# Performance work log

Measured on AMD Instinct MI355X. Metric: run time of the kernel, lower is better.

Reference implementation:

```python
import jax, jax.numpy as jnp
import numpy as np

B, N, D = 2, 2048, 1024
H, HD = 16, 64


def setup_inputs() -> dict:
    key = jax.random.key(0)
    ks = jax.random.split(key, 5)
    return {
        "hidden_states": jax.random.normal(ks[0], (B, N, D), dtype=jnp.float32),
        "W_attn": jax.random.normal(ks[1], (D, 3 * D), dtype=jnp.float32) * (D ** -0.5),
        "b_attn": jax.random.normal(ks[2], (3 * D,), dtype=jnp.float32) * 0.02,
        "W_proj": jax.random.normal(ks[3], (D, D), dtype=jnp.float32) * (D ** -0.5),
        "b_proj": jax.random.normal(ks[4], (D,), dtype=jnp.float32) * 0.02,
    }


def reference(hidden_states, W_attn, b_attn, W_proj, b_proj):
    # QKV projection: [B,N,3D]
    proj = hidden_states @ W_attn + b_attn
    q, k, v = jnp.split(proj, 3, axis=-1)
    # [B,N,H,HD]
    q = q.reshape(B, N, H, HD)
    k = k.reshape(B, N, H, HD)
    v = v.reshape(B, N, H, HD)
    scale = HD ** -0.5
    # naive attention: full [B,H,Nq,Nkv] score matrix
    attn = jnp.einsum("bqhd,bkhd->bhqk", q, k) * scale
    q_pos = jnp.arange(N)
    kv_pos = jnp.arange(N)
    # mask where kv_pos > start_pos + q_pos (start_pos = 0)
    mask = kv_pos[None, :] > q_pos[:, None]  # [Nq, Nkv]
    attn = jnp.where(mask[None, None, :, :], -jnp.inf, attn)
    attn = jax.nn.softmax(attn, axis=-1)
    out = jnp.einsum("bhqk,bkhd->bqhd", attn, v)  # [B,N,H,HD]
    out = out.reshape(B, N, D)
    return out @ W_proj + b_proj
```

## Files before the change

### kernel.cpp

```cpp
#include <hip/hip_runtime.h>
#include <hip/hip_bf16.h>

#define BB 2
#define NN 2048
#define DDIM 1024
#define HH 16
#define HDD 64

typedef __attribute__((ext_vector_type(8))) short bf16x8;
typedef __attribute__((ext_vector_type(4))) short bf16x4;
typedef __attribute__((ext_vector_type(4))) float f32x4;

__device__ inline ushort f2bf(float x) {
  __hip_bfloat16 h = __float2bfloat16(x);
  ushort u;
  __builtin_memcpy(&u, &h, 2);
  return u;
}

#define GLOAD_LDS16(g, l)                                                            \
  __builtin_amdgcn_global_load_lds((const __attribute__((address_space(1))) void*)(g), \
                                   (__attribute__((address_space(3))) void*)(l), 16, 0, 0)

__global__ __launch_bounds__(256) void cvt_f32_bf16(const float* __restrict__ in,
                                                    ushort* __restrict__ out, int n4) {
  int i = blockIdx.x * 256 + threadIdx.x;
  if (i >= n4) return;
  float4 a = ((const float4*)in)[i];
  ushort4 o;
  o.x = f2bf(a.x); o.y = f2bf(a.y); o.z = f2bf(a.z); o.w = f2bf(a.w);
  ((ushort4*)out)[i] = o;
}

__global__ __launch_bounds__(256) void transpose_cvt(const float* __restrict__ in,
                                                     ushort* __restrict__ out, int R, int C) {
  __shared__ float tile[32][33];
  int bx = blockIdx.x * 32, by = blockIdx.y * 32;
  int tx = threadIdx.x, ty = threadIdx.y;
#pragma unroll
  for (int r = ty; r < 32; r += 8)
    tile[r][tx] = in[(size_t)(by + r) * C + bx + tx];
  __syncthreads();
#pragma unroll
  for (int r = ty; r < 32; r += 8)
    out[(size_t)(bx + r) * R + by + tx] = f2bf(tile[tx][r]);
}

template <int MODE>
__global__ __launch_bounds__(256) void gemm_bt(const ushort* __restrict__ A,
                                               const ushort* __restrict__ Bt,
                                               const float* __restrict__ bias,
                                               void* __restrict__ Cv,
                                               ushort* __restrict__ Vt,
                                               int M, int N, int K) {
  __shared__ ushort As[128 * 32];
  __shared__ ushort Bs[128 * 32];
  const int tid = threadIdx.x;
  const int wid = tid >> 6, lane = tid & 63;
  const int c = lane & 15, g = lane >> 4;
  const int wm = (wid >> 1) * 64, wn = (wid & 1) * 64;
  const int m0 = blockIdx.y * 128, n0 = blockIdx.x * 128;
  f32x4 acc[4][4] = {};
  for (int k0 = 0; k0 < K; k0 += 32) {
    __syncthreads();
#pragma unroll
    for (int it = 0; it < 2; ++it) {
      int G = tid + it * 256;
      int row = G >> 2, sl = G & 3;
      GLOAD_LDS16(A + (size_t)(m0 + row) * K + k0 + sl * 8, &As[G * 8]);
      GLOAD_LDS16(Bt + (size_t)(n0 + row) * K + k0 + sl * 8, &Bs[G * 8]);
    }
    __syncthreads();
    bf16x8 af[4], bfr[4];
#pragma unroll
    for (int i = 0; i < 4; ++i) {
      af[i] = *(const bf16x8*)(&As[(wm + i * 16 + c) * 32 + g * 8]);
      bfr[i] = *(const bf16x8*)(&Bs[(wn + i * 16 + c) * 32 + g * 8]);
    }
#pragma unroll
    for (int i = 0; i < 4; ++i)
#pragma unroll
      for (int j = 0; j < 4; ++j)
        acc[i][j] = __builtin_amdgcn_mfma_f32_16x16x32_bf16(af[i], bfr[j], acc[i][j], 0, 0, 0);
  }
#pragma unroll
  for (int i = 0; i < 4; ++i) {
#pragma unroll
    for (int j = 0; j < 4; ++j) {
      const int col = n0 + wn + j * 16 + c;
      const float bv = bias[col];
      const int row = m0 + wm + i * 16 + g * 4;
      if (MODE == 2 && col >= 2048) {
        const int hh = (col - 2048) >> 6, dd = (col - 2048) & 63;
        const int bb = row >> 11, nl = row & 2047;
        ushort4 ov;
        ov.x = f2bf(acc[i][j][0] + bv);
        ov.y = f2bf(acc[i][j][1] + bv);
        ov.z = f2bf(acc[i][j][2] + bv);
        ov.w = f2bf(acc[i][j][3] + bv);
        *(ushort4*)(&Vt[(size_t)((bb * 16 + hh) * 64 + dd) * NN + nl]) = ov;
      } else {
        const int ldc = (MODE == 2) ? 2048 : N;
#pragma unroll
        for (int ri = 0; ri < 4; ++ri) {
          float v = acc[i][j][ri] + bv;
          if (MODE == 0)
            ((float*)Cv)[(size_t)(row + ri) * ldc + col] = v;
          else
            ((ushort*)Cv)[(size_t)(row + ri) * ldc + col] = f2bf(v);
        }
      }
    }
  }
}

__global__ __launch_bounds__(256) void attn_fwd(const ushort* __restrict__ QK,
                                                const ushort* __restrict__ Vt,
                                                ushort* __restrict__ O) {
  const int bh = blockIdx.x;
  const int b = bh >> 4, h = bh & 15;
  const int qb = (int)gridDim.y - 1 - (int)blockIdx.y;
  const int tid = threadIdx.x;
  const int wid = tid >> 6, lane = tid & 63;
  const int c = lane & 15, g = lane >> 4;
  const int q0 = qb * 64 + wid * 16;
  const ushort* Qb = QK + (size_t)b * NN * 2048 + (size_t)h * HDD;
  const ushort* Kb = Qb + 1024;
  const ushort* Vb = Vt + (size_t)bh * HDD * NN;

  __shared__ ushort Ks[64 * 64];
  __shared__ ushort Vs[64 * 64];

  bf16x8 qf[2];
  {
    const ushort* qrow = Qb + (size_t)(q0 + c) * 2048 + g * 8;
    qf[0] = *(const bf16x8*)(qrow);
    qf[1] = *(const bf16x8*)(qrow + 32);
  }
  f32x4 oacc[4] = {};
  float m = -INFINITY, lsum = 0.f;
  const int q_abs = q0 + c;
  const int ntiles = qb + 1;

  for (int t = 0; t < ntiles; ++t) {
    const int kv0 = t * 64;
    __syncthreads();
#pragma unroll
    for (int it = 0; it < 2; ++it) {
      int u = tid + it * 256;
      int row = u >> 3, sl = u & 7;
      *(bf16x8*)(&Ks[row * 64 + ((sl ^ (row & 7)) * 8)]) =
          *(const bf16x8*)(Kb + (size_t)(kv0 + row) * 2048 + sl * 8);
      *(bf16x8*)(&Vs[row * 64 + ((sl ^ (row & 7)) * 8)]) =
          *(const bf16x8*)(Vb + (size_t)row * NN + kv0 + sl * 8);
    }
    __syncthreads();

    f32x4 s[4] = {};
#pragma unroll
    for (int f = 0; f < 4; ++f) {
      int krow = f * 16 + c;
#pragma unroll
      for (int dc = 0; dc < 2; ++dc) {
        int slot = dc * 4 + g;
        bf16x8 kf = *(const bf16x8*)(&Ks[krow * 64 + ((slot ^ (krow & 7)) * 8)]);
        s[f] = __builtin_amdgcn_mfma_f32_16x16x32_bf16(kf, qf[dc], s[f], 0, 0, 0);
      }
    }

    float pmax = -INFINITY;
#pragma unroll
    for (int f = 0; f < 4; ++f)
#pragma unroll
      for (int i = 0; i < 4; ++i) {
        int kv_abs = kv0 + f * 16 + g * 4 + i;
        float sv = (kv_abs > q_abs) ? -INFINITY : s[f][i] * 0.125f;
        s[f][i] = sv;
        pmax = fmaxf(pmax, sv);
      }
    pmax = fmaxf(pmax, __shfl_xor(pmax, 16));
    pmax = fmaxf(pmax, __shfl_xor(pmax, 32));
    float mnew = fmaxf(m, pmax);
    float corr = __expf(m - mnew);
    float psum = 0.f;
#pragma unroll
    for (int f = 0; f < 4; ++f)
#pragma unroll
      for (int i = 0; i < 4; ++i) {
        float p = __expf(s[f][i] - mnew);
        s[f][i] = p;
        psum += p;
      }
    psum += __shfl_xor(psum, 16);
    psum += __shfl_xor(psum, 32);
    lsum = lsum * corr + psum;
    m = mnew;
#pragma unroll
    for (int db = 0; db < 4; ++db) {
      oacc[db][0] *= corr; oacc[db][1] *= corr;
      oacc[db][2] *= corr; oacc[db][3] *= corr;
    }

#pragma unroll
    for (int f = 0; f < 4; ++f) {
      bf16x4 pb;
      pb[0] = (short)f2bf(s[f][0]);
      pb[1] = (short)f2bf(s[f][1]);
      pb[2] = (short)f2bf(s[f][2]);
      pb[3] = (short)f2bf(s[f][3]);
      const int slot = f * 2 + (g >> 1);
#pragma unroll
      for (int db = 0; db < 4; ++db) {
        int d = db * 16 + c;
        bf16x4 vf = *(const bf16x4*)(&Vs[d * 64 + ((slot ^ (d & 7)) * 8) + (g & 1) * 4]);
        oacc[db] = __builtin_amdgcn_mfma_f32_16x16x16bf16_1k(vf, pb, oacc[db], 0, 0, 0);
      }
    }
  }

  float invl = 1.f / lsum;
  ushort* orow = O + (size_t)(b * NN + q0 + c) * DDIM + h * HDD;
#pragma unroll
  for (int db = 0; db < 4; ++db) {
    ushort4 ov;
    ov.x = f2bf(oacc[db][0] * invl);
    ov.y = f2bf(oacc[db][1] * invl);
    ov.z = f2bf(oacc[db][2] * invl);
    ov.w = f2bf(oacc[db][3] * invl);
    *(ushort4*)(&orow[db * 16 + g * 4]) = ov;
  }
}

extern "C" void kernel_launch(void* const* d_in, const int* in_sizes, int n_in,
                              void* d_out, int out_size, void* d_ws, size_t ws_size,
                              hipStream_t stream) {
  const float* hidden = (const float*)d_in[0];
  const float* W_attn = (const float*)d_in[1];
  const float* b_attn = (const float*)d_in[2];
  const float* W_proj = (const float*)d_in[3];
  const float* b_proj = (const float*)d_in[4];

  char* ws = (char*)d_ws;
  ushort* hbf  = (ushort*)(ws);
  ushort* WaT  = (ushort*)(ws + (size_t)(8 << 20));
  ushort* WpT  = (ushort*)(ws + (size_t)(14 << 20));
  ushort* qk   = (ushort*)(ws + (size_t)(16 << 20));
  ushort* vt   = (ushort*)(ws + (size_t)(32 << 20));
  ushort* aout = (ushort*)(ws + (size_t)(40 << 20));

  cvt_f32_bf16<<<4096, 256, 0, stream>>>(hidden, hbf, (BB * NN * DDIM) / 4);
  transpose_cvt<<<dim3(96, 32), dim3(32, 8), 0, stream>>>(W_attn, WaT, 1024, 3072);
  transpose_cvt<<<dim3(32, 32), dim3(32, 8), 0, stream>>>(W_proj, WpT, 1024, 1024);

  gemm_bt<2><<<dim3(24, 32), 256, 0, stream>>>(hbf, WaT, b_attn, qk, vt, 4096, 3072, 1024);
  attn_fwd<<<dim3(32, 32), 256, 0, stream>>>(qk, vt, aout);
  gemm_bt<0><<<dim3(8, 32), 256, 0, stream>>>(aout, WpT, b_proj, d_out, nullptr, 4096, 1024, 1024);
}
```

Measured before the change: 230.1 us.

## Double-buffer attention K/V via direct LDS loads, lazy softmax rescale, new proj GEMM

The attention kernel now double-buffers K/V tiles in LDS using global_load_lds, so the next tile loads while the current one is computed, and drops one barrier per iteration. The softmax folds scale·log2e into Q, uses raw exp2, applies the causal mask only on the diagonal tile, skips rescaling unless the running max grows by more than a threshold, and defers the row-sum shuffles to the end. The output projection moves to a dedicated 64x128-tile GEMM kernel with twice the blocks. Pre-rounding Q to bf16 after scaling, and letting the max lag by up to 8 in log2 units, change numerics slightly and could overflow in rare cases.

```diff
diff --git a/kernel.cpp b/kernel.cpp
--- a/kernel.cpp
+++ b/kernel.cpp
@@ -17,8 +17,19 @@
   __builtin_memcpy(&u, &h, 2);
   return u;
 }
-
-#define GLOAD_LDS16(g, l)                                                            \
+__device__ inline float bf2f(ushort u) {
+  unsigned v = (unsigned)u << 16;
+  float f;
+  __builtin_memcpy(&f, &v, 4);
+  return f;
+}
+__device__ inline float exp2_raw(float x) {
+  float r;
+  asm("v_exp_f32 %0, %1" : "=v"(r) : "v"(x));
+  return r;
+}
+
+#define GLOAD_LDS16(g, l)                                                              \
   __builtin_amdgcn_global_load_lds((const __attribute__((address_space(1))) void*)(g), \
                                    (__attribute__((address_space(3))) void*)(l), 16, 0, 0)
 
@@ -104,12 +115,62 @@
 #pragma unroll
         for (int ri = 0; ri < 4; ++ri) {
           float v = acc[i][j][ri] + bv;
-          if (MODE == 0)
-            ((float*)Cv)[(size_t)(row + ri) * ldc + col] = v;
-          else
-            ((ushort*)Cv)[(size_t)(row + ri) * ldc + col] = f2bf(v);
+          ((ushort*)Cv)[(size_t)(row + ri) * ldc + col] = f2bf(v);
         }
       }
+    }
+  }
+}
+
+__global__ __launch_bounds__(256) void gemm_proj(const ushort* __restrict__ A,
+                                                 const ushort* __restrict__ Bt,
+                                                 const float* __restrict__ bias,
+                                                 float* __restrict__ C, int M, int N, int K) {
+  __shared__ ushort As[64 * 32];
+  __shared__ ushort Bs[128 * 32];
+  const int tid = threadIdx.x;
+  const int wid = tid >> 6, lane = tid & 63;
+  const int c = lane & 15, g = lane >> 4;
+  const int wn = wid * 32;
+  const int m0 = blockIdx.y * 64, n0 = blockIdx.x * 128;
+  f32x4 acc[4][2] = {};
+  for (int k0 = 0; k0 < K; k0 += 32) {
+    __syncthreads();
+#pragma unroll
+    for (int it = 0; it < 3; ++it) {
+      int G = tid + it * 256;
+      if (G < 256) {
+        int row = G >> 2, sl = G & 3;
+        GLOAD_LDS16(A + (size_t)(m0 + row) * K + k0 + sl * 8, &As[G * 8]);
+      } else {
+        int GB = G - 256;
+        int row = GB >> 2, sl = GB & 3;
+        GLOAD_LDS16(Bt + (size_t)(n0 + row) * K + k0 + sl * 8, &Bs[GB * 8]);
+      }
+    }
+    __syncthreads();
+    bf16x8 af[4], bfr[2];
+#pragma unroll
+    for (int i = 0; i < 4; ++i) af[i] = *(const bf16x8*)(&As[(i * 16 + c) * 32 + g * 8]);
+#pragma unroll
+    for (int j = 0; j < 2; ++j)
+      bfr[j] = *(const bf16x8*)(&Bs[(wn + j * 16 + c) * 32 + g * 8]);
+#pragma unroll
+    for (int i = 0; i < 4; ++i)
+#pragma unroll
+      for (int j = 0; j < 2; ++j)
+        acc[i][j] = __builtin_amdgcn_mfma_f32_16x16x32_bf16(af[i], bfr[j], acc[i][j], 0, 0, 0);
+  }
+#pragma unroll
+  for (int i = 0; i < 4; ++i) {
+#pragma unroll
+    for (int j = 0; j < 2; ++j) {
+      const int col = n0 + wn + j * 16 + c;
+      const float bv = bias[col];
+      const int row = m0 + i * 16 + g * 4;
+#pragma unroll
+      for (int ri = 0; ri < 4; ++ri)
+        C[(size_t)(row + ri) * N + col] = acc[i][j][ri] + bv;
     }
   }
 }
@@ -128,33 +189,42 @@
   const ushort* Kb = Qb + 1024;
   const ushort* Vb = Vt + (size_t)bh * HDD * NN;
 
-  __shared__ ushort Ks[64 * 64];
-  __shared__ ushort Vs[64 * 64];
-
+  __shared__ ushort Ks[2][64 * 64];
+  __shared__ ushort Vs[2][64 * 64];
+
+  const float SC = 0.18033688011112042f;
   bf16x8 qf[2];
   {
     const ushort* qrow = Qb + (size_t)(q0 + c) * 2048 + g * 8;
     qf[0] = *(const bf16x8*)(qrow);
     qf[1] = *(const bf16x8*)(qrow + 32);
-  }
+#pragma unroll
+    for (int r = 0; r < 2; ++r)
+#pragma unroll
+      for (int e = 0; e < 8; ++e) qf[r][e] = (short)f2bf(bf2f((ushort)qf[r][e]) * SC);
+  }
+
   f32x4 oacc[4] = {};
-  float m = -INFINITY, lsum = 0.f;
+  float m = 0.f, lsum = 0.f;
   const int q_abs = q0 + c;
-  const int ntiles = qb + 1;
-
-  for (int t = 0; t < ntiles; ++t) {
-    const int kv0 = t * 64;
-    __syncthreads();
-#pragma unroll
-    for (int it = 0; it < 2; ++it) {
-      int u = tid + it * 256;
-      int row = u >> 3, sl = u & 7;
-      *(bf16x8*)(&Ks[row * 64 + ((sl ^ (row & 7)) * 8)]) =
-          *(const bf16x8*)(Kb + (size_t)(kv0 + row) * 2048 + sl * 8);
-      *(bf16x8*)(&Vs[row * 64 + ((sl ^ (row & 7)) * 8)]) =
-          *(const bf16x8*)(Vb + (size_t)row * NN + kv0 + sl * 8);
-    }
-    __syncthreads();
+
+#define STAGE_TILE(kv0, bufi)                                                   \
+  do {                                                                          \
+    _Pragma("unroll") for (int it = 0; it < 2; ++it) {                          \
+      int u = tid + it * 256;                                                   \
+      int row = u >> 3, sl = u & 7;                                             \
+      int ksl = (sl ^ (row & 7)) * 8;                                           \
+      GLOAD_LDS16(Kb + (size_t)((kv0) + row) * 2048 + ksl, &Ks[bufi][u * 8]);   \
+      GLOAD_LDS16(Vb + (size_t)row * NN + (kv0) + ksl, &Vs[bufi][u * 8]);       \
+    }                                                                           \
+  } while (0)
+
+  STAGE_TILE(0, 0);
+  __syncthreads();
+  int cur = 0;
+
+  for (int t = 0; t <= qb; ++t) {
+    if (t < qb) STAGE_TILE((t + 1) * 64, cur ^ 1);
 
     f32x4 s[4] = {};
 #pragma unroll
@@ -162,44 +232,57 @@
       int krow = f * 16 + c;
 #pragma unroll
       for (int dc = 0; dc < 2; ++dc) {
-        int slot = dc * 4 + g;
-        bf16x8 kf = *(const bf16x8*)(&Ks[krow * 64 + ((slot ^ (krow & 7)) * 8)]);
+        int slot = (dc * 4 + g) ^ (krow & 7);
+        bf16x8 kf = *(const bf16x8*)(&Ks[cur][krow * 64 + slot * 8]);
         s[f] = __builtin_amdgcn_mfma_f32_16x16x32_bf16(kf, qf[dc], s[f], 0, 0, 0);
       }
     }
 
     float pmax = -INFINITY;
+    if (t == qb) {
+      const int kv0 = t * 64;
+#pragma unroll
+      for (int f = 0; f < 4; ++f)
+#pragma unroll
+        for (int i = 0; i < 4; ++i) {
+          if (kv0 + f * 16 + g * 4 + i > q_abs) s[f][i] = -INFINITY;
+          pmax = fmaxf(pmax, s[f][i]);
+        }
+    } else {
+#pragma unroll
+      for (int f = 0; f < 4; ++f)
+#pragma unroll
+        for (int i = 0; i < 4; ++i) pmax = fmaxf(pmax, s[f][i]);
+    }
+
+    if (t == 0) {
+      float pr = fmaxf(pmax, __shfl_xor(pmax, 16));
+      pr = fmaxf(pr, __shfl_xor(pr, 32));
+      m = pr;
+    } else if (!__all(pmax <= m + 8.f)) {
+      float pr = fmaxf(pmax, __shfl_xor(pmax, 16));
+      pr = fmaxf(pr, __shfl_xor(pr, 32));
+      float mnew = fmaxf(m, pr);
+      float corr = exp2_raw(m - mnew);
+      lsum *= corr;
+#pragma unroll
+      for (int db = 0; db < 4; ++db) {
+        oacc[db][0] *= corr; oacc[db][1] *= corr;
+        oacc[db][2] *= corr; oacc[db][3] *= corr;
+      }
+      m = mnew;
+    }
+
+    float psum = 0.f;
 #pragma unroll
     for (int f = 0; f < 4; ++f)
 #pragma unroll
       for (int i = 0; i < 4; ++i) {
-        int kv_abs = kv0 + f * 16 + g * 4 + i;
-        float sv = (kv_abs > q_abs) ? -INFINITY : s[f][i] * 0.125f;
-        s[f][i] = sv;
-        pmax = fmaxf(pmax, sv);
-      }
-    pmax = fmaxf(pmax, __shfl_xor(pmax, 16));
-    pmax = fmaxf(pmax, __shfl_xor(pmax, 32));
-    float mnew = fmaxf(m, pmax);
-    float corr = __expf(m - mnew);
-    float psum = 0.f;
-#pragma unroll
-    for (int f = 0; f < 4; ++f)
-#pragma unroll
-      for (int i = 0; i < 4; ++i) {
-        float p = __expf(s[f][i] - mnew);
+        float p = exp2_raw(s[f][i] - m);
         s[f][i] = p;
         psum += p;
       }
-    psum += __shfl_xor(psum, 16);
-    psum += __shfl_xor(psum, 32);
-    lsum = lsum * corr + psum;
-    m = mnew;
-#pragma unroll
-    for (int db = 0; db < 4; ++db) {
-      oacc[db][0] *= corr; oacc[db][1] *= corr;
-      oacc[db][2] *= corr; oacc[db][3] *= corr;
-    }
+    lsum += psum;
 
 #pragma unroll
     for (int f = 0; f < 4; ++f) {
@@ -212,12 +295,17 @@
 #pragma unroll
       for (int db = 0; db < 4; ++db) {
         int d = db * 16 + c;
-        bf16x4 vf = *(const bf16x4*)(&Vs[d * 64 + ((slot ^ (d & 7)) * 8) + (g & 1) * 4]);
+        bf16x4 vf =
+            *(const bf16x4*)(&Vs[cur][d * 64 + ((slot ^ (d & 7)) * 8) + (g & 1) * 4]);
         oacc[db] = __builtin_amdgcn_mfma_f32_16x16x16bf16_1k(vf, pb, oacc[db], 0, 0, 0);
       }
     }
-  }
-
+    __syncthreads();
+    cur ^= 1;
+  }
+
+  lsum += __shfl_xor(lsum, 16);
+  lsum += __shfl_xor(lsum, 32);
   float invl = 1.f / lsum;
   ushort* orow = O + (size_t)(b * NN + q0 + c) * DDIM + h * HDD;
 #pragma unroll
@@ -254,5 +342,5 @@
 
   gemm_bt<2><<<dim3(24, 32), 256, 0, stream>>>(hbf, WaT, b_attn, qk, vt, 4096, 3072, 1024);
   attn_fwd<<<dim3(32, 32), 256, 0, stream>>>(qk, vt, aout);
-  gemm_bt<0><<<dim3(8, 32), 256, 0, stream>>>(aout, WpT, b_proj, d_out, nullptr, 4096, 1024, 1024);
-}
+  gemm_proj<<<dim3(8, 64), 256, 0, stream>>>(aout, WpT, b_proj, (float*)d_out, 4096, 1024, 1024);
+}
```

Result: faster. 191.0 us (-17.0%).
